# Optimization experiments

Measured on AMD Instinct MI355X. Metric: run time of the kernel, lower is better.

## Reference

```python
import jax, jax.numpy as jnp
import numpy as np

V, D, DEPTH, L, H, DH, FF = 32000, 1024, 4, 2048, 16, 64, 4096
INNER = H * DH
EPS = 1e-5


def ln(x, g, b):
    m = jnp.mean(x, axis=-1, keepdims=True)
    v = jnp.mean(jnp.square(x - m), axis=-1, keepdims=True)
    return (x - m) * jax.lax.rsqrt(v + EPS) * g + b


def setup_inputs() -> dict:
    key = jax.random.key(0)
    ks = jax.random.split(key, 16)
    s = 0.02
    inp = {
        'x': jax.random.randint(ks[0], (1, L), 0, V),
        'tok_emb': jax.random.normal(ks[1], (V, D), jnp.float32) * s,
        'pos_emb': jax.random.normal(ks[2], (L, D), jnp.float32) * s,
        'attn_ng': jnp.ones((DEPTH, D), jnp.float32),
        'attn_nb': jnp.zeros((DEPTH, D), jnp.float32),
        'wqkv': jax.random.normal(ks[3], (DEPTH, D, 3 * INNER), jnp.float32) * s,
        'wo': jax.random.normal(ks[4], (DEPTH, INNER, D), jnp.float32) * s,
        'bo': jnp.zeros((DEPTH, D), jnp.float32),
        'out_ng': jnp.ones((DEPTH, D), jnp.float32),
        'out_nb': jnp.zeros((DEPTH, D), jnp.float32),
        'ff_ng': jnp.ones((DEPTH, D), jnp.float32),
        'ff_nb': jnp.zeros((DEPTH, D), jnp.float32),
        'w1': jax.random.normal(ks[5], (DEPTH, D, FF), jnp.float32) * s,
        'b1': jnp.zeros((DEPTH, FF), jnp.float32),
        'w2': jax.random.normal(ks[6], (DEPTH, FF, D), jnp.float32) * s,
        'b2': jnp.zeros((DEPTH, D), jnp.float32),
        'fin_g': jnp.ones((D,), jnp.float32),
        'fin_b': jnp.zeros((D,), jnp.float32),
        'w_logit': jax.random.normal(ks[7], (D, V), jnp.float32) * s,
        'b_logit': jnp.zeros((V,), jnp.float32),
    }
    return inp


def reference(x, tok_emb, pos_emb, attn_ng, attn_nb, wqkv, wo, bo, out_ng, out_nb,
              ff_ng, ff_nb, w1, b1, w2, b2, fin_g, fin_b, w_logit, b_logit):
    n = x.shape[1]
    scale = DH ** -0.5
    # causal keep-mask: j <= i (lower triangular incl diagonal)
    causal = jnp.tril(jnp.ones((n, n), bool))
    h = tok_emb[x] + pos_emb[:n][None]  # [b, n, D]
    for l in range(DEPTH):
        # --- ReLA attention ---
        y = ln(h, attn_ng[l], attn_nb[l])
        qkv = y @ wqkv[l]  # [b, n, 3*INNER]
        q, k, v = jnp.split(qkv, 3, axis=-1)
        q = q.reshape(-1, n, H, DH).transpose(0, 2, 1, 3) * scale  # [b,H,n,d]
        k = k.reshape(-1, n, H, DH).transpose(0, 2, 1, 3)
        v = v.reshape(-1, n, H, DH).transpose(0, 2, 1, 3)
        sim = jnp.einsum('bhid,bhjd->bhij', q, k)
        attn = jnp.where(causal, jax.nn.relu(sim), 0.0)  # mask then ReLU
        o = jnp.einsum('bhij,bhjd->bhid', attn, v)
        o = o.transpose(0, 2, 1, 3).reshape(-1, n, INNER)  # [b,n,INNER]
        o = ln(o @ wo[l] + bo[l], out_ng[l], out_nb[l])
        h = o + h
        # --- FFN ---
        y = ln(h, ff_ng[l], ff_nb[l])
        y = jax.nn.gelu(y @ w1[l] + b1[l], approximate=False) @ w2[l] + b2[l]
        h = y + h
    return ln(h, fin_g, fin_b) @ w_logit + b_logit
```

## Files before the change

kernel.cpp:

```cpp
#include <hip/hip_runtime.h>
#include <hip/hip_bf16.h>
#include <math.h>

#define SEQ   2048
#define DM    1024
#define NH    16
#define DHD   64
#define FFD   4096
#define NV    32000

typedef __bf16 bf16x8 __attribute__((ext_vector_type(8)));
typedef float  f32x4  __attribute__((ext_vector_type(4)));

typedef __attribute__((address_space(1))) void* gas_ptr;
typedef __attribute__((address_space(3))) void* las_ptr;

static __device__ __forceinline__ void gload16(const void* g, void* l) {
  __builtin_amdgcn_global_load_lds((gas_ptr)g, (las_ptr)l, 16, 0, 0);
}

static __device__ __forceinline__ unsigned short f2bf(float f) {
  unsigned int x = __float_as_uint(f);
  return (unsigned short)((x + 0x7fffu + ((x >> 16) & 1u)) >> 16);
}

static __device__ __forceinline__ bf16x8 ld_frag(const unsigned short* p) {
  union { uint4 u; bf16x8 v; } r;
  r.u = *(const uint4*)p;
  return r.v;
}

__global__ __launch_bounds__(256)
void k_transpose_bf16(const float* __restrict__ in, unsigned short* __restrict__ out,
                      int K, int N, size_t lstride) {
  in  += (size_t)blockIdx.z * lstride;
  out += (size_t)blockIdx.z * lstride;
  __shared__ float tl[64 * 65];
  const int bk = blockIdx.x * 64, bn = blockIdx.y * 64;
  const int t = threadIdx.x;
  const int tx = t & 15, ty = t >> 4;
#pragma unroll
  for (int i = 0; i < 4; ++i) {
    const int r = i * 16 + ty;
    float4 v = *(const float4*)&in[(size_t)(bk + r) * N + bn + tx * 4];
    tl[(tx * 4 + 0) * 65 + r] = v.x;
    tl[(tx * 4 + 1) * 65 + r] = v.y;
    tl[(tx * 4 + 2) * 65 + r] = v.z;
    tl[(tx * 4 + 3) * 65 + r] = v.w;
  }
  __syncthreads();
#pragma unroll
  for (int j = 0; j < 2; ++j) {
    const int f = j * 256 + t;
    const int n = f >> 3, kc = (f & 7) * 8;
    union { unsigned short u[8]; uint4 v; } pk;
#pragma unroll
    for (int e = 0; e < 8; ++e) pk.u[e] = f2bf(tl[n * 65 + kc + e]);
    *(uint4*)&out[(size_t)(bn + n) * K + bk + kc] = pk.v;
  }
}

__global__ __launch_bounds__(256)
void k_vT(const unsigned short* __restrict__ qkv, unsigned short* __restrict__ vT) {
  __shared__ unsigned short tile[32][33];
  const int bs = blockIdx.x * 32, bd = blockIdx.y * 32;
  const int tx = threadIdx.x & 31, ty = threadIdx.x >> 5;
#pragma unroll
  for (int r = ty; r < 32; r += 8)
    tile[r][tx] = qkv[(size_t)(bs + r) * (3 * DM) + 2 * DM + bd + tx];
  __syncthreads();
#pragma unroll
  for (int r = ty; r < 32; r += 8)
    vT[(size_t)(bd + r) * SEQ + bs + tx] = tile[tx][r];
}

__global__ __launch_bounds__(256)
void k_embed(const int* __restrict__ x, const float* __restrict__ tok,
             const float* __restrict__ pos, float* __restrict__ h) {
  const int row = blockIdx.x;
  const int d = threadIdx.x * 4;
  const int tk = x[row];
  float4 a = *(const float4*)(tok + (size_t)tk * DM + d);
  float4 p = *(const float4*)(pos + (size_t)row * DM + d);
  float4 o; o.x = a.x + p.x; o.y = a.y + p.y; o.z = a.z + p.z; o.w = a.w + p.w;
  *(float4*)(h + (size_t)row * DM + d) = o;
}

__global__ __launch_bounds__(256)
void k_ln_bf16(const float* __restrict__ in, const float* __restrict__ g,
               const float* __restrict__ b, unsigned short* __restrict__ out) {
  const int row = blockIdx.x, t = threadIdx.x;
  float4 v = *(const float4*)(in + (size_t)row * DM + t * 4);
  float s = v.x + v.y + v.z + v.w;
  float q = v.x * v.x + v.y * v.y + v.z * v.z + v.w * v.w;
#pragma unroll
  for (int o = 32; o; o >>= 1) { s += __shfl_xor(s, o); q += __shfl_xor(q, o); }
  __shared__ float ls[4], lq[4];
  if ((t & 63) == 0) { ls[t >> 6] = s; lq[t >> 6] = q; }
  __syncthreads();
  s = ls[0] + ls[1] + ls[2] + ls[3];
  q = lq[0] + lq[1] + lq[2] + lq[3];
  const float mean = s * (1.f / DM);
  const float rstd = rsqrtf(q * (1.f / DM) - mean * mean + 1e-5f);
  float4 gg = *(const float4*)(g + t * 4);
  float4 bb = *(const float4*)(b + t * 4);
  ushort4 o4;
  o4.x = f2bf((v.x - mean) * rstd * gg.x + bb.x);
  o4.y = f2bf((v.y - mean) * rstd * gg.y + bb.y);
  o4.z = f2bf((v.z - mean) * rstd * gg.z + bb.z);
  o4.w = f2bf((v.w - mean) * rstd * gg.w + bb.w);
  *(ushort4*)(out + (size_t)row * DM + t * 4) = o4;
}

__global__ __launch_bounds__(256)
void k_addslab_ln_ln(float* __restrict__ h, const float* __restrict__ sl,
                     const float* __restrict__ bo,
                     const float* __restrict__ g1, const float* __restrict__ b1,
                     const float* __restrict__ g2, const float* __restrict__ b2,
                     unsigned short* __restrict__ out) {
  const int row = blockIdx.x, t = threadIdx.x;
  __shared__ float ls[4], lq[4], ls2[4], lq2[4];
  const size_t idx = (size_t)row * DM + t * 4;
  float4 v = *(const float4*)(bo + t * 4);
#pragma unroll
  for (int c = 0; c < 4; ++c) {
    float4 p = *(const float4*)(sl + (size_t)c * SEQ * DM + idx);
    v.x += p.x; v.y += p.y; v.z += p.z; v.w += p.w;
  }
  float s = v.x + v.y + v.z + v.w;
  float q = v.x * v.x + v.y * v.y + v.z * v.z + v.w * v.w;
#pragma unroll
  for (int o = 32; o; o >>= 1) { s += __shfl_xor(s, o); q += __shfl_xor(q, o); }
  if ((t & 63) == 0) { ls[t >> 6] = s; lq[t >> 6] = q; }
  __syncthreads();
  s = ls[0] + ls[1] + ls[2] + ls[3];
  q = lq[0] + lq[1] + lq[2] + lq[3];
  const float mean = s * (1.f / DM);
  const float rstd = rsqrtf(q * (1.f / DM) - mean * mean + 1e-5f);
  float4 gg = *(const float4*)(g1 + t * 4);
  float4 bb = *(const float4*)(b1 + t * 4);
  float4 hv = *(const float4*)(h + idx);
  hv.x += (v.x - mean) * rstd * gg.x + bb.x;
  hv.y += (v.y - mean) * rstd * gg.y + bb.y;
  hv.z += (v.z - mean) * rstd * gg.z + bb.z;
  hv.w += (v.w - mean) * rstd * gg.w + bb.w;
  *(float4*)(h + idx) = hv;
  float s2 = hv.x + hv.y + hv.z + hv.w;
  float q2 = hv.x * hv.x + hv.y * hv.y + hv.z * hv.z + hv.w * hv.w;
#pragma unroll
  for (int o = 32; o; o >>= 1) { s2 += __shfl_xor(s2, o); q2 += __shfl_xor(q2, o); }
  if ((t & 63) == 0) { ls2[t >> 6] = s2; lq2[t >> 6] = q2; }
  __syncthreads();
  s2 = ls2[0] + ls2[1] + ls2[2] + ls2[3];
  q2 = lq2[0] + lq2[1] + lq2[2] + lq2[3];
  const float mean2 = s2 * (1.f / DM);
  const float rstd2 = rsqrtf(q2 * (1.f / DM) - mean2 * mean2 + 1e-5f);
  float4 g2v = *(const float4*)(g2 + t * 4);
  float4 b2v = *(const float4*)(b2 + t * 4);
  ushort4 o4;
  o4.x = f2bf((hv.x - mean2) * rstd2 * g2v.x + b2v.x);
  o4.y = f2bf((hv.y - mean2) * rstd2 * g2v.y + b2v.y);
  o4.z = f2bf((hv.z - mean2) * rstd2 * g2v.z + b2v.z);
  o4.w = f2bf((hv.w - mean2) * rstd2 * g2v.w + b2v.w);
  *(ushort4*)(out + (size_t)row * DM + t * 4) = o4;
}

__global__ __launch_bounds__(256)
void k_redadd_ln(float* __restrict__ h, const float* __restrict__ sl,
                 const float* __restrict__ b2,
                 const float* __restrict__ g, const float* __restrict__ b,
                 unsigned short* __restrict__ out) {
  const int row = blockIdx.x, t = threadIdx.x;
  __shared__ float ls[4], lq[4];
  const size_t idx = (size_t)row * DM + t * 4;
  float4 hv = *(const float4*)(h + idx);
  float4 bb = *(const float4*)(b2 + t * 4);
  hv.x += bb.x; hv.y += bb.y; hv.z += bb.z; hv.w += bb.w;
#pragma unroll
  for (int c = 0; c < 4; ++c) {
    float4 p = *(const float4*)(sl + (size_t)c * SEQ * DM + idx);
    hv.x += p.x; hv.y += p.y; hv.z += p.z; hv.w += p.w;
  }
  *(float4*)(h + idx) = hv;
  float s = hv.x + hv.y + hv.z + hv.w;
  float q = hv.x * hv.x + hv.y * hv.y + hv.z * hv.z + hv.w * hv.w;
#pragma unroll
  for (int o = 32; o; o >>= 1) { s += __shfl_xor(s, o); q += __shfl_xor(q, o); }
  if ((t & 63) == 0) { ls[t >> 6] = s; lq[t >> 6] = q; }
  __syncthreads();
  s = ls[0] + ls[1] + ls[2] + ls[3];
  q = lq[0] + lq[1] + lq[2] + lq[3];
  const float mean = s * (1.f / DM);
  const float rstd = rsqrtf(q * (1.f / DM) - mean * mean + 1e-5f);
  float4 gg = *(const float4*)(g + t * 4);
  float4 b1 = *(const float4*)(b + t * 4);
  ushort4 o4;
  o4.x = f2bf((hv.x - mean) * rstd * gg.x + b1.x);
  o4.y = f2bf((hv.y - mean) * rstd * gg.y + b1.y);
  o4.z = f2bf((hv.z - mean) * rstd * gg.z + b1.z);
  o4.w = f2bf((hv.w - mean) * rstd * gg.w + b1.w);
  *(ushort4*)(out + (size_t)row * DM + t * 4) = o4;
}

template<int EPI>
__global__ __launch_bounds__(512, 1)
void k_gemm2(const unsigned short* __restrict__ A, const unsigned short* __restrict__ Bt,
             float* __restrict__ outF, unsigned short* __restrict__ outB,
             const float* __restrict__ bias, int N, int K, int kLen, int gm) {
  __shared__ __align__(16) unsigned short L[49152];
  const int nwg = gridDim.x, pid = blockIdx.x;
  const int qq = nwg >> 3, rr = nwg & 7;
  const int xcd = pid & 7, lo = pid >> 3;
  const int wg = ((xcd < rr) ? xcd * (qq + 1) : rr * (qq + 1) + (xcd - rr) * qq) + lo;
  const int bm = wg % gm, bn = wg / gm;
  const int kOff = blockIdx.y * kLen;
  const int t = threadIdx.x, lane = t & 63, w = t >> 6;
  const int wm = w >> 2, wn = w & 3, lr = lane & 15, lg = lane >> 4;

  const unsigned short* gA[2]; unsigned short* lA[2];
  const unsigned short* gB[4]; unsigned short* lB[4];
#pragma unroll
  for (int j = 0; j < 2; ++j) {
    const int f = j * 512 + t, row = f >> 3, c = f & 7;
    gA[j] = A + (size_t)(bm * 128 + row) * K + kOff + ((c ^ (row & 7)) << 3);
    lA[j] = L + f * 8;
  }
#pragma unroll
  for (int j = 0; j < 4; ++j) {
    const int f = j * 512 + t, row = f >> 3, c = f & 7;
    gB[j] = Bt + (size_t)(bn * 256 + row) * K + kOff + ((c ^ (row & 7)) << 3);
    lB[j] = L + 16384 + f * 8;
  }
  auto stage = [&](int k0, int c) {
#pragma unroll
    for (int j = 0; j < 2; ++j) gload16(gA[j] + k0, lA[j] + c * 8192);
#pragma unroll
    for (int j = 0; j < 4; ++j) gload16(gB[j] + k0, lB[j] + c * 16384);
  };

  int offA[4][2], offB[4][2];
#pragma unroll
  for (int mt = 0; mt < 4; ++mt)
#pragma unroll
    for (int ks = 0; ks < 2; ++ks) {
      const int rowA = wm * 64 + mt * 16 + lr;
      offA[mt][ks] = rowA * 64 + (((ks * 4 + lg) ^ (rowA & 7)) << 3);
      const int rowB = wn * 64 + mt * 16 + lr;
      offB[mt][ks] = rowB * 64 + (((ks * 4 + lg) ^ (rowB & 7)) << 3);
    }

  const f32x4 zero = {0.f, 0.f, 0.f, 0.f};
  f32x4 acc[4][4];
#pragma unroll
  for (int i = 0; i < 4; ++i)
#pragma unroll
    for (int j = 0; j < 4; ++j) acc[i][j] = zero;

  const int NT = kLen >> 6;
  stage(0, 0);
  if (NT > 1) stage(64, 1);

  for (int tt = 0; tt < NT; ++tt) {
    const int c = tt & 1;
    if (tt + 1 < NT) asm volatile("s_waitcnt vmcnt(6)" ::: "memory");
    else             asm volatile("s_waitcnt vmcnt(0)" ::: "memory");
    __builtin_amdgcn_s_barrier();
    const unsigned short* Ab = L + c * 8192;
    const unsigned short* Bb = L + 16384 + c * 16384;
    bf16x8 af[4][2], bfr[4][2];
#pragma unroll
    for (int mt = 0; mt < 4; ++mt)
#pragma unroll
      for (int ks = 0; ks < 2; ++ks) {
        af[mt][ks]  = ld_frag(Ab + offA[mt][ks]);
        bfr[mt][ks] = ld_frag(Bb + offB[mt][ks]);
      }
    __builtin_amdgcn_s_setprio(1);
#pragma unroll
    for (int ks = 0; ks < 2; ++ks)
#pragma unroll
      for (int mt = 0; mt < 4; ++mt)
#pragma unroll
        for (int nt = 0; nt < 4; ++nt)
          acc[mt][nt] = __builtin_amdgcn_mfma_f32_16x16x32_bf16(af[mt][ks], bfr[nt][ks], acc[mt][nt], 0, 0, 0);
    __builtin_amdgcn_s_setprio(0);
    __builtin_amdgcn_s_barrier();
    if (tt + 2 < NT) stage((tt + 2) << 6, c);
  }

  const int rbase = bm * 128 + wm * 64;
  const int cbase = bn * 256 + wn * 64;
  float* outP = outF;
  if constexpr (EPI == 4) outP = outF + (size_t)blockIdx.y * SEQ * N;
#pragma unroll
  for (int mt = 0; mt < 4; ++mt) {
#pragma unroll
    for (int nt = 0; nt < 4; ++nt) {
      const int col = cbase + nt * 16 + lr;
      float bv = 0.f;
      if constexpr (EPI == 1 || EPI == 2) bv = bias[col];
#pragma unroll
      for (int r = 0; r < 4; ++r) {
        const int row = rbase + mt * 16 + lg * 4 + r;
        float v = acc[mt][nt][r] + bv;
        if constexpr (EPI == 2) v = 0.5f * v * (1.f + erff(v * 0.70710678118f));
        if constexpr (EPI == 0 || EPI == 2) outB[(size_t)row * N + col] = f2bf(v);
        else                                outP[(size_t)row * N + col] = v;
      }
    }
  }
}

__global__ __launch_bounds__(256)
void k_gemm4(const unsigned short* __restrict__ A, const unsigned short* __restrict__ Bt,
             float* __restrict__ outF, const float* __restrict__ bias,
             int N, int K, int gm) {
  __shared__ __align__(16) unsigned short L[16384];
  const int nwg = gridDim.x, pid = blockIdx.x;
  const int qq = nwg >> 3, rr = nwg & 7;
  const int xcd = pid & 7, lo = pid >> 3;
  const int wg = ((xcd < rr) ? xcd * (qq + 1) : rr * (qq + 1) + (xcd - rr) * qq) + lo;
  const int bm = wg % gm, bn = wg / gm;
  const int t = threadIdx.x, lane = t & 63, w = t >> 6;
  const int wm = w >> 1, wn = w & 1, lr = lane & 15, lg = lane >> 4;

  const unsigned short* gA[2]; const unsigned short* gB[2];
  unsigned short* lA[2]; unsigned short* lB[2];
#pragma unroll
  for (int j = 0; j < 2; ++j) {
    const int f = j * 256 + t;
    const int row = f >> 2;
    const int c = (f & 3) ^ (row & 3);
    gA[j] = A  + (size_t)(bm * 128 + row) * K + c * 8;
    gB[j] = Bt + (size_t)(bn * 128 + row) * K + c * 8;
    lA[j] = L + f * 8;
    lB[j] = L + 4096 + f * 8;
  }
  auto stage = [&](int k0, int cb) {
#pragma unroll
    for (int j = 0; j < 2; ++j) gload16(gA[j] + k0, lA[j] + cb * 8192);
#pragma unroll
    for (int j = 0; j < 2; ++j) gload16(gB[j] + k0, lB[j] + cb * 8192);
  };

  int offA[4], offB[4];
#pragma unroll
  for (int mt = 0; mt < 4; ++mt) {
    const int rowA = wm * 64 + mt * 16 + lr;
    offA[mt] = rowA * 32 + ((lg ^ (rowA & 3)) << 3);
    const int rowB = wn * 64 + mt * 16 + lr;
    offB[mt] = 4096 + rowB * 32 + ((lg ^ (rowB & 3)) << 3);
  }

  f32x4 acc[4][4];
#pragma unroll
  for (int i = 0; i < 4; ++i)
#pragma unroll
    for (int j = 0; j < 4; ++j) acc[i][j] = (f32x4){0.f, 0.f, 0.f, 0.f};

  const int NT = K >> 5;
  stage(0, 0);
  stage(32, 1);

  for (int tt = 0; tt < NT; ++tt) {
    const int cb = tt & 1;
    if (tt + 1 < NT) asm volatile("s_waitcnt vmcnt(4)" ::: "memory");
    else             asm volatile("s_waitcnt vmcnt(0)" ::: "memory");
    __builtin_amdgcn_s_barrier();
    const unsigned short* buf = L + cb * 8192;
    bf16x8 af[4], bfr[4];
#pragma unroll
    for (int mt = 0; mt < 4; ++mt) {
      af[mt]  = ld_frag(buf + offA[mt]);
      bfr[mt] = ld_frag(buf + offB[mt]);
    }
    __builtin_amdgcn_s_setprio(1);
#pragma unroll
    for (int mt = 0; mt < 4; ++mt)
#pragma unroll
      for (int nt = 0; nt < 4; ++nt)
        acc[mt][nt] = __builtin_amdgcn_mfma_f32_16x16x32_bf16(af[mt], bfr[nt], acc[mt][nt], 0, 0, 0);
    __builtin_amdgcn_s_setprio(0);
    __builtin_amdgcn_s_barrier();
    if (tt + 2 < NT) stage((tt + 2) << 5, cb);
  }

  const int rbase = bm * 128 + wm * 64;
  const int cbase = bn * 128 + wn * 64;
#pragma unroll
  for (int mt = 0; mt < 4; ++mt) {
#pragma unroll
    for (int nt = 0; nt < 4; ++nt) {
      const int col = cbase + nt * 16 + lr;
      const float bv = bias[col];
#pragma unroll
      for (int r = 0; r < 4; ++r) {
        const int row = rbase + mt * 16 + lg * 4 + r;
        outF[(size_t)row * N + col] = acc[mt][nt][r] + bv;
      }
    }
  }
}

__global__ __launch_bounds__(256)
void k_rela_attn(const unsigned short* __restrict__ qkv,
                 const unsigned short* __restrict__ vT,
                 unsigned short* __restrict__ obf) {
  const int jb = blockIdx.x;
  const int hd = blockIdx.y;
  const int qbA = jb, qbB = 31 - jb;
  const int t = threadIdx.x, lane = t & 63, w = t >> 6;
  const int lr = lane & 15, lg = lane >> 4;

  __shared__ __align__(16) unsigned short Qs[128 * 64];
  __shared__ __align__(16) unsigned short Ks[64 * 64];
  __shared__ __align__(16) unsigned short Vs[64 * 64];
  __shared__ __align__(16) unsigned short Ps[4][16 * 72];

  const int sr8 = lane >> 3;
  const int sch = ((lane & 7) ^ sr8) << 3;

#pragma unroll
  for (int qi = 0; qi < 4; ++qi) {
    const int i = w * 4 + qi;
    const int rl = i * 8 + sr8;
    const int grow = (rl < 64) ? (qbA * 64 + rl) : (qbB * 64 + rl - 64);
    gload16(qkv + (size_t)grow * (3 * DM) + hd * DHD + sch, Qs + i * 512);
  }
  __syncthreads();

  bf16x8 qfA[2], qfB[2];
#pragma unroll
  for (int ks = 0; ks < 2; ++ks) {
    const int rowA = w * 16 + lr;
    qfA[ks] = ld_frag(&Qs[rowA * 64 + (((ks * 4 + lg) ^ (lr & 7)) << 3)]);
    const int rowB = 64 + w * 16 + lr;
    qfB[ks] = ld_frag(&Qs[rowB * 64 + (((ks * 4 + lg) ^ (lr & 7)) << 3)]);
  }

  const f32x4 zero = {0.f, 0.f, 0.f, 0.f};
  f32x4 accA[4], accB[4];
#pragma unroll
  for (int nt = 0; nt < 4; ++nt) { accA[nt] = zero; accB[nt] = zero; }

  auto tile_step = [&](const bf16x8* qf, f32x4* acc, int qb, int kt) {
    f32x4 sv[4];
#pragma unroll
    for (int nt = 0; nt < 4; ++nt) sv[nt] = zero;
#pragma unroll
    for (int ks = 0; ks < 2; ++ks)
#pragma unroll
      for (int nt = 0; nt < 4; ++nt) {
        bf16x8 kf = ld_frag(&Ks[(nt * 16 + lr) * 64 + (((ks * 4 + lg) ^ (lr & 7)) << 3)]);
        sv[nt] = __builtin_amdgcn_mfma_f32_16x16x32_bf16(qf[ks], kf, sv[nt], 0, 0, 0);
      }
    const bool diag = (kt == qb);
#pragma unroll
    for (int nt = 0; nt < 4; ++nt)
#pragma unroll
      for (int r = 0; r < 4; ++r) {
        float v = fmaxf(sv[nt][r], 0.f) * 0.125f;
        if (diag) {
          const int ii = w * 16 + lg * 4 + r;
          const int jj = nt * 16 + lr;
          if (jj > ii) v = 0.f;
        }
        Ps[w][(lg * 4 + r) * 72 + nt * 16 + lr] = f2bf(v);
      }
#pragma unroll
    for (int ks = 0; ks < 2; ++ks) {
      bf16x8 pf = ld_frag(&Ps[w][lr * 72 + ks * 32 + lg * 8]);
#pragma unroll
      for (int nt = 0; nt < 4; ++nt) {
        bf16x8 vf = ld_frag(&Vs[(nt * 16 + lr) * 64 + (((ks * 4 + lg) ^ (lr & 7)) << 3)]);
        acc[nt] = __builtin_amdgcn_mfma_f32_16x16x32_bf16(pf, vf, acc[nt], 0, 0, 0);
      }
    }
  };

  for (int kt = 0; kt <= qbB; ++kt) {
    __syncthreads();
#pragma unroll
    for (int qi = 0; qi < 2; ++qi) {
      const int i = w * 2 + qi;
      const int rl = i * 8 + sr8;
      gload16(qkv + (size_t)(kt * 64 + rl) * (3 * DM) + DM + hd * DHD + sch, Ks + i * 512);
      gload16(vT + (size_t)(hd * DHD + rl) * SEQ + kt * 64 + sch, Vs + i * 512);
    }
    __syncthreads();
    tile_step(qfB, accB, qbB, kt);
    if (kt <= qbA) tile_step(qfA, accA, qbA, kt);
  }

#pragma unroll
  for (int nt = 0; nt < 4; ++nt)
#pragma unroll
    for (int r = 0; r < 4; ++r) {
      const int col = hd * DHD + nt * 16 + lr;
      const int rowA = qbA * 64 + w * 16 + lg * 4 + r;
      obf[(size_t)rowA * DM + col] = f2bf(accA[nt][r]);
      const int rowB = qbB * 64 + w * 16 + lg * 4 + r;
      obf[(size_t)rowB * DM + col] = f2bf(accB[nt][r]);
    }
}

extern "C" void kernel_launch(void* const* d_in, const int* in_sizes, int n_in,
                              void* d_out, int out_size, void* d_ws, size_t ws_size,
                              hipStream_t stream) {
  const int*   x       = (const int*)d_in[0];
  const float* tok_emb = (const float*)d_in[1];
  const float* pos_emb = (const float*)d_in[2];
  const float* attn_ng = (const float*)d_in[3];
  const float* attn_nb = (const float*)d_in[4];
  const float* wqkv    = (const float*)d_in[5];
  const float* wo      = (const float*)d_in[6];
  const float* bo      = (const float*)d_in[7];
  const float* out_ng  = (const float*)d_in[8];
  const float* out_nb  = (const float*)d_in[9];
  const float* ff_ng   = (const float*)d_in[10];
  const float* ff_nb   = (const float*)d_in[11];
  const float* w1      = (const float*)d_in[12];
  const float* b1      = (const float*)d_in[13];
  const float* w2      = (const float*)d_in[14];
  const float* b2      = (const float*)d_in[15];
  const float* fin_g   = (const float*)d_in[16];
  const float* fin_b   = (const float*)d_in[17];
  const float* w_logit = (const float*)d_in[18];
  const float* b_logit = (const float*)d_in[19];
  float* out = (float*)d_out;

  char* ws = (char*)d_ws;
  size_t off = 0;
  auto alloc = [&](size_t bytes) -> void* {
    void* p = ws + off;
    off = (off + bytes + 255) & ~(size_t)255;
    return p;
  };
  unsigned short* wqkvT = (unsigned short*)alloc(4ull * 3072 * 1024 * 2);
  unsigned short* woT   = (unsigned short*)alloc(4ull * 1024 * 1024 * 2);
  unsigned short* w1T   = (unsigned short*)alloc(4ull * 4096 * 1024 * 2);
  unsigned short* w2T   = (unsigned short*)alloc(4ull * 1024 * 4096 * 2);
  unsigned short* wlogT = (unsigned short*)alloc((size_t)NV * 1024 * 2);
  float*          h     = (float*)alloc((size_t)SEQ * DM * 4);
  unsigned short* ybf   = (unsigned short*)alloc((size_t)SEQ * DM * 2);
  unsigned short* qkvbf = (unsigned short*)alloc((size_t)SEQ * 3 * DM * 2);
  unsigned short* vTb   = (unsigned short*)alloc((size_t)DM * SEQ * 2);
  unsigned short* obf   = (unsigned short*)alloc((size_t)SEQ * DM * 2);
  unsigned short* ffbf  = (unsigned short*)alloc((size_t)SEQ * FFD * 2);
  float*          slabs = (float*)alloc(4ull * SEQ * DM * 4);
  (void)ws_size; (void)in_sizes; (void)n_in; (void)out_size;

  const dim3 B(256);
  const dim3 G2(512);

  k_transpose_bf16<<<dim3(16, 48, 4), B, 0, stream>>>(wqkv, wqkvT, 1024, 3072, (size_t)1024 * 3072);
  k_transpose_bf16<<<dim3(16, 16, 4), B, 0, stream>>>(wo, woT, 1024, 1024, (size_t)1024 * 1024);
  k_transpose_bf16<<<dim3(16, 64, 4), B, 0, stream>>>(w1, w1T, 1024, 4096, (size_t)1024 * 4096);
  k_transpose_bf16<<<dim3(64, 16, 4), B, 0, stream>>>(w2, w2T, 4096, 1024, (size_t)4096 * 1024);
  k_transpose_bf16<<<dim3(16, 500, 1), B, 0, stream>>>(w_logit, wlogT, 1024, NV, 0);

  k_embed<<<SEQ, B, 0, stream>>>(x, tok_emb, pos_emb, h);
  k_ln_bf16<<<SEQ, B, 0, stream>>>(h, attn_ng, attn_nb, ybf);

  for (int l = 0; l < 4; ++l) {
    k_gemm2<0><<<dim3(192), G2, 0, stream>>>(
        ybf, wqkvT + (size_t)l * 3072 * 1024, nullptr, qkvbf, nullptr, 3072, 1024, 1024, 16);
    k_vT<<<dim3(SEQ / 32, DM / 32), B, 0, stream>>>(qkvbf, vTb);
    k_rela_attn<<<dim3(16, NH), B, 0, stream>>>(qkvbf, vTb, obf);
    k_gemm2<4><<<dim3(64, 4), G2, 0, stream>>>(
        obf, woT + (size_t)l * 1024 * 1024, slabs, nullptr, nullptr, 1024, 1024, 256, 16);
    k_addslab_ln_ln<<<SEQ, B, 0, stream>>>(h, slabs, bo + l * DM,
                                           out_ng + l * DM, out_nb + l * DM,
                                           ff_ng + l * DM, ff_nb + l * DM, ybf);
    k_gemm2<2><<<dim3(256), G2, 0, stream>>>(
        ybf, w1T + (size_t)l * 4096 * 1024, nullptr, ffbf, b1 + l * FFD, 4096, 1024, 1024, 16);
    k_gemm2<4><<<dim3(64, 4), G2, 0, stream>>>(
        ffbf, w2T + (size_t)l * 1024 * 4096, slabs, nullptr, nullptr, 1024, 4096, 1024, 16);
    const float* ng = (l < 3) ? (attn_ng + (l + 1) * DM) : fin_g;
    const float* nb = (l < 3) ? (attn_nb + (l + 1) * DM) : fin_b;
    k_redadd_ln<<<SEQ, B, 0, stream>>>(h, slabs, b2 + l * DM, ng, nb, ybf);
  }

  k_gemm4<<<dim3(4000), B, 0, stream>>>(ybf, wlogT, out, b_logit, NV, 1024, 16);
}
```

Before: 1.028 ms.

## Unify GEMMs on 128x128 tile kernel and split attention KV range across two blocks

Replaces the 512-thread 128x256 GEMM with a templated 256-thread 128x128 kernel (BK=32, new swizzle) used by every layer GEMM and the logit projection. The attention kernel is split along the key dimension into two z-slices with double-buffered K/V staging. Each slice writes fp32 partial outputs, and a new kernel sums them into bf16. This aims to balance work and raise occupancy, at the cost of an extra reduction kernel, fp32 slab traffic, and smaller GEMM tiles with less reuse.

```diff
diff --git a/kernel.cpp b/kernel.cpp
--- a/kernel.cpp
+++ b/kernel.cpp
@@ -110,6 +110,20 @@
   o4.z = f2bf((v.z - mean) * rstd * gg.z + bb.z);
   o4.w = f2bf((v.w - mean) * rstd * gg.w + bb.w);
   *(ushort4*)(out + (size_t)row * DM + t * 4) = o4;
+}
+
+__global__ __launch_bounds__(256)
+void k_ored(const float* __restrict__ sl, unsigned short* __restrict__ obf) {
+  const int row = blockIdx.x, t = threadIdx.x;
+  const size_t idx = (size_t)row * DM + t * 4;
+  float4 a = *(const float4*)(sl + idx);
+  float4 b = *(const float4*)(sl + (size_t)SEQ * DM + idx);
+  ushort4 o4;
+  o4.x = f2bf(a.x + b.x);
+  o4.y = f2bf(a.y + b.y);
+  o4.z = f2bf(a.z + b.z);
+  o4.w = f2bf(a.w + b.w);
+  *(ushort4*)(obf + idx) = o4;
 }
 
 __global__ __launch_bounds__(256)
@@ -203,11 +217,11 @@
 }
 
 template<int EPI>
-__global__ __launch_bounds__(512, 1)
-void k_gemm2(const unsigned short* __restrict__ A, const unsigned short* __restrict__ Bt,
+__global__ __launch_bounds__(256)
+void k_gemm4(const unsigned short* __restrict__ A, const unsigned short* __restrict__ Bt,
              float* __restrict__ outF, unsigned short* __restrict__ outB,
              const float* __restrict__ bias, int N, int K, int kLen, int gm) {
-  __shared__ __align__(16) unsigned short L[49152];
+  __shared__ __align__(16) unsigned short L[16384];
   const int nwg = gridDim.x, pid = blockIdx.x;
   const int qq = nwg >> 3, rr = nwg & 7;
   const int xcd = pid & 7, lo = pid >> 3;
@@ -215,81 +229,71 @@
   const int bm = wg % gm, bn = wg / gm;
   const int kOff = blockIdx.y * kLen;
   const int t = threadIdx.x, lane = t & 63, w = t >> 6;
-  const int wm = w >> 2, wn = w & 3, lr = lane & 15, lg = lane >> 4;
-
-  const unsigned short* gA[2]; unsigned short* lA[2];
-  const unsigned short* gB[4]; unsigned short* lB[4];
+  const int wm = w >> 1, wn = w & 1, lr = lane & 15, lg = lane >> 4;
+
+  const unsigned short* gA[2]; const unsigned short* gB[2];
+  unsigned short* lA[2]; unsigned short* lB[2];
 #pragma unroll
   for (int j = 0; j < 2; ++j) {
-    const int f = j * 512 + t, row = f >> 3, c = f & 7;
-    gA[j] = A + (size_t)(bm * 128 + row) * K + kOff + ((c ^ (row & 7)) << 3);
+    const int f = j * 256 + t;
+    const int row = f >> 2;
+    const int c = (f & 3) ^ ((row >> 1) & 3);
+    gA[j] = A  + (size_t)(bm * 128 + row) * K + kOff + c * 8;
+    gB[j] = Bt + (size_t)(bn * 128 + row) * K + kOff + c * 8;
     lA[j] = L + f * 8;
-  }
-#pragma unroll
-  for (int j = 0; j < 4; ++j) {
-    const int f = j * 512 + t, row = f >> 3, c = f & 7;
-    gB[j] = Bt + (size_t)(bn * 256 + row) * K + kOff + ((c ^ (row & 7)) << 3);
-    lB[j] = L + 16384 + f * 8;
-  }
-  auto stage = [&](int k0, int c) {
-#pragma unroll
-    for (int j = 0; j < 2; ++j) gload16(gA[j] + k0, lA[j] + c * 8192);
-#pragma unroll
-    for (int j = 0; j < 4; ++j) gload16(gB[j] + k0, lB[j] + c * 16384);
+    lB[j] = L + 4096 + f * 8;
+  }
+  auto stage = [&](int k0, int cb) {
+#pragma unroll
+    for (int j = 0; j < 2; ++j) gload16(gA[j] + k0, lA[j] + cb * 8192);
+#pragma unroll
+    for (int j = 0; j < 2; ++j) gload16(gB[j] + k0, lB[j] + cb * 8192);
   };
 
-  int offA[4][2], offB[4][2];
-#pragma unroll
-  for (int mt = 0; mt < 4; ++mt)
-#pragma unroll
-    for (int ks = 0; ks < 2; ++ks) {
-      const int rowA = wm * 64 + mt * 16 + lr;
-      offA[mt][ks] = rowA * 64 + (((ks * 4 + lg) ^ (rowA & 7)) << 3);
-      const int rowB = wn * 64 + mt * 16 + lr;
-      offB[mt][ks] = rowB * 64 + (((ks * 4 + lg) ^ (rowB & 7)) << 3);
-    }
-
-  const f32x4 zero = {0.f, 0.f, 0.f, 0.f};
+  int offA[4], offB[4];
+#pragma unroll
+  for (int mt = 0; mt < 4; ++mt) {
+    const int rowA = wm * 64 + mt * 16 + lr;
+    offA[mt] = rowA * 32 + ((lg ^ ((rowA >> 1) & 3)) << 3);
+    const int rowB = wn * 64 + mt * 16 + lr;
+    offB[mt] = 4096 + rowB * 32 + ((lg ^ ((rowB >> 1) & 3)) << 3);
+  }
+
   f32x4 acc[4][4];
 #pragma unroll
   for (int i = 0; i < 4; ++i)
 #pragma unroll
-    for (int j = 0; j < 4; ++j) acc[i][j] = zero;
-
-  const int NT = kLen >> 6;
+    for (int j = 0; j < 4; ++j) acc[i][j] = (f32x4){0.f, 0.f, 0.f, 0.f};
+
+  const int NT = kLen >> 5;
   stage(0, 0);
-  if (NT > 1) stage(64, 1);
+  stage(32, 1);
 
   for (int tt = 0; tt < NT; ++tt) {
-    const int c = tt & 1;
-    if (tt + 1 < NT) asm volatile("s_waitcnt vmcnt(6)" ::: "memory");
+    const int cb = tt & 1;
+    if (tt + 1 < NT) asm volatile("s_waitcnt vmcnt(4)" ::: "memory");
     else             asm volatile("s_waitcnt vmcnt(0)" ::: "memory");
     __builtin_amdgcn_s_barrier();
-    const unsigned short* Ab = L + c * 8192;
-    const unsigned short* Bb = L + 16384 + c * 16384;
-    bf16x8 af[4][2], bfr[4][2];
+    const unsigned short* buf = L + cb * 8192;
+    bf16x8 af[4], bfr[4];
+#pragma unroll
+    for (int mt = 0; mt < 4; ++mt) {
+      af[mt]  = ld_frag(buf + offA[mt]);
+      bfr[mt] = ld_frag(buf + offB[mt]);
+    }
+    __builtin_amdgcn_s_setprio(1);
 #pragma unroll
     for (int mt = 0; mt < 4; ++mt)
 #pragma unroll
-      for (int ks = 0; ks < 2; ++ks) {
-        af[mt][ks]  = ld_frag(Ab + offA[mt][ks]);
-        bfr[mt][ks] = ld_frag(Bb + offB[mt][ks]);
-      }
-    __builtin_amdgcn_s_setprio(1);
-#pragma unroll
-    for (int ks = 0; ks < 2; ++ks)
-#pragma unroll
-      for (int mt = 0; mt < 4; ++mt)
-#pragma unroll
-        for (int nt = 0; nt < 4; ++nt)
-          acc[mt][nt] = __builtin_amdgcn_mfma_f32_16x16x32_bf16(af[mt][ks], bfr[nt][ks], acc[mt][nt], 0, 0, 0);
+      for (int nt = 0; nt < 4; ++nt)
+        acc[mt][nt] = __builtin_amdgcn_mfma_f32_16x16x32_bf16(af[mt], bfr[nt], acc[mt][nt], 0, 0, 0);
     __builtin_amdgcn_s_setprio(0);
     __builtin_amdgcn_s_barrier();
-    if (tt + 2 < NT) stage((tt + 2) << 6, c);
+    if (tt + 2 < NT) stage((tt + 2) << 5, cb);
   }
 
   const int rbase = bm * 128 + wm * 64;
-  const int cbase = bn * 256 + wn * 64;
+  const int cbase = bn * 128 + wn * 64;
   float* outP = outF;
   if constexpr (EPI == 4) outP = outF + (size_t)blockIdx.y * SEQ * N;
 #pragma unroll
@@ -312,109 +316,20 @@
 }
 
 __global__ __launch_bounds__(256)
-void k_gemm4(const unsigned short* __restrict__ A, const unsigned short* __restrict__ Bt,
-             float* __restrict__ outF, const float* __restrict__ bias,
-             int N, int K, int gm) {
-  __shared__ __align__(16) unsigned short L[16384];
-  const int nwg = gridDim.x, pid = blockIdx.x;
-  const int qq = nwg >> 3, rr = nwg & 7;
-  const int xcd = pid & 7, lo = pid >> 3;
-  const int wg = ((xcd < rr) ? xcd * (qq + 1) : rr * (qq + 1) + (xcd - rr) * qq) + lo;
-  const int bm = wg % gm, bn = wg / gm;
-  const int t = threadIdx.x, lane = t & 63, w = t >> 6;
-  const int wm = w >> 1, wn = w & 1, lr = lane & 15, lg = lane >> 4;
-
-  const unsigned short* gA[2]; const unsigned short* gB[2];
-  unsigned short* lA[2]; unsigned short* lB[2];
-#pragma unroll
-  for (int j = 0; j < 2; ++j) {
-    const int f = j * 256 + t;
-    const int row = f >> 2;
-    const int c = (f & 3) ^ (row & 3);
-    gA[j] = A  + (size_t)(bm * 128 + row) * K + c * 8;
-    gB[j] = Bt + (size_t)(bn * 128 + row) * K + c * 8;
-    lA[j] = L + f * 8;
-    lB[j] = L + 4096 + f * 8;
-  }
-  auto stage = [&](int k0, int cb) {
-#pragma unroll
-    for (int j = 0; j < 2; ++j) gload16(gA[j] + k0, lA[j] + cb * 8192);
-#pragma unroll
-    for (int j = 0; j < 2; ++j) gload16(gB[j] + k0, lB[j] + cb * 8192);
-  };
-
-  int offA[4], offB[4];
-#pragma unroll
-  for (int mt = 0; mt < 4; ++mt) {
-    const int rowA = wm * 64 + mt * 16 + lr;
-    offA[mt] = rowA * 32 + ((lg ^ (rowA & 3)) << 3);
-    const int rowB = wn * 64 + mt * 16 + lr;
-    offB[mt] = 4096 + rowB * 32 + ((lg ^ (rowB & 3)) << 3);
-  }
-
-  f32x4 acc[4][4];
-#pragma unroll
-  for (int i = 0; i < 4; ++i)
-#pragma unroll
-    for (int j = 0; j < 4; ++j) acc[i][j] = (f32x4){0.f, 0.f, 0.f, 0.f};
-
-  const int NT = K >> 5;
-  stage(0, 0);
-  stage(32, 1);
-
-  for (int tt = 0; tt < NT; ++tt) {
-    const int cb = tt & 1;
-    if (tt + 1 < NT) asm volatile("s_waitcnt vmcnt(4)" ::: "memory");
-    else             asm volatile("s_waitcnt vmcnt(0)" ::: "memory");
-    __builtin_amdgcn_s_barrier();
-    const unsigned short* buf = L + cb * 8192;
-    bf16x8 af[4], bfr[4];
-#pragma unroll
-    for (int mt = 0; mt < 4; ++mt) {
-      af[mt]  = ld_frag(buf + offA[mt]);
-      bfr[mt] = ld_frag(buf + offB[mt]);
-    }
-    __builtin_amdgcn_s_setprio(1);
-#pragma unroll
-    for (int mt = 0; mt < 4; ++mt)
-#pragma unroll
-      for (int nt = 0; nt < 4; ++nt)
-        acc[mt][nt] = __builtin_amdgcn_mfma_f32_16x16x32_bf16(af[mt], bfr[nt], acc[mt][nt], 0, 0, 0);
-    __builtin_amdgcn_s_setprio(0);
-    __builtin_amdgcn_s_barrier();
-    if (tt + 2 < NT) stage((tt + 2) << 5, cb);
-  }
-
-  const int rbase = bm * 128 + wm * 64;
-  const int cbase = bn * 128 + wn * 64;
-#pragma unroll
-  for (int mt = 0; mt < 4; ++mt) {
-#pragma unroll
-    for (int nt = 0; nt < 4; ++nt) {
-      const int col = cbase + nt * 16 + lr;
-      const float bv = bias[col];
-#pragma unroll
-      for (int r = 0; r < 4; ++r) {
-        const int row = rbase + mt * 16 + lg * 4 + r;
-        outF[(size_t)row * N + col] = acc[mt][nt][r] + bv;
-      }
-    }
-  }
-}
-
-__global__ __launch_bounds__(256)
 void k_rela_attn(const unsigned short* __restrict__ qkv,
                  const unsigned short* __restrict__ vT,
-                 unsigned short* __restrict__ obf) {
+                 float* __restrict__ osl) {
   const int jb = blockIdx.x;
   const int hd = blockIdx.y;
+  const int z  = blockIdx.z;
   const int qbA = jb, qbB = 31 - jb;
+  const int ha = (qbA + 2) >> 1, hb = (qbB + 2) >> 1;
   const int t = threadIdx.x, lane = t & 63, w = t >> 6;
   const int lr = lane & 15, lg = lane >> 4;
 
   __shared__ __align__(16) unsigned short Qs[128 * 64];
-  __shared__ __align__(16) unsigned short Ks[64 * 64];
-  __shared__ __align__(16) unsigned short Vs[64 * 64];
+  __shared__ __align__(16) unsigned short Ks[2][64 * 64];
+  __shared__ __align__(16) unsigned short Vs[2][64 * 64];
   __shared__ __align__(16) unsigned short Ps[4][16 * 72];
 
   const int sr8 = lane >> 3;
@@ -443,7 +358,17 @@
 #pragma unroll
   for (int nt = 0; nt < 4; ++nt) { accA[nt] = zero; accB[nt] = zero; }
 
-  auto tile_step = [&](const bf16x8* qf, f32x4* acc, int qb, int kt) {
+  auto stage = [&](int kt, int cb) {
+#pragma unroll
+    for (int qi = 0; qi < 2; ++qi) {
+      const int i = w * 2 + qi;
+      const int rl = i * 8 + sr8;
+      gload16(qkv + (size_t)(kt * 64 + rl) * (3 * DM) + DM + hd * DHD + sch, &Ks[cb][i * 512]);
+      gload16(vT + (size_t)(hd * DHD + rl) * SEQ + kt * 64 + sch, &Vs[cb][i * 512]);
+    }
+  };
+
+  auto tile_step = [&](const bf16x8* qf, f32x4* acc, int qb, int kt, int cb) {
     f32x4 sv[4];
 #pragma unroll
     for (int nt = 0; nt < 4; ++nt) sv[nt] = zero;
@@ -451,7 +376,7 @@
     for (int ks = 0; ks < 2; ++ks)
 #pragma unroll
       for (int nt = 0; nt < 4; ++nt) {
-        bf16x8 kf = ld_frag(&Ks[(nt * 16 + lr) * 64 + (((ks * 4 + lg) ^ (lr & 7)) << 3)]);
+        bf16x8 kf = ld_frag(&Ks[cb][(nt * 16 + lr) * 64 + (((ks * 4 + lg) ^ (lr & 7)) << 3)]);
         sv[nt] = __builtin_amdgcn_mfma_f32_16x16x32_bf16(qf[ks], kf, sv[nt], 0, 0, 0);
       }
     const bool diag = (kt == qb);
@@ -472,35 +397,47 @@
       bf16x8 pf = ld_frag(&Ps[w][lr * 72 + ks * 32 + lg * 8]);
 #pragma unroll
       for (int nt = 0; nt < 4; ++nt) {
-        bf16x8 vf = ld_frag(&Vs[(nt * 16 + lr) * 64 + (((ks * 4 + lg) ^ (lr & 7)) << 3)]);
+        bf16x8 vf = ld_frag(&Vs[cb][(nt * 16 + lr) * 64 + (((ks * 4 + lg) ^ (lr & 7)) << 3)]);
         acc[nt] = __builtin_amdgcn_mfma_f32_16x16x32_bf16(pf, vf, acc[nt], 0, 0, 0);
       }
     }
   };
 
-  for (int kt = 0; kt <= qbB; ++kt) {
-    __syncthreads();
-#pragma unroll
-    for (int qi = 0; qi < 2; ++qi) {
-      const int i = w * 2 + qi;
-      const int rl = i * 8 + sr8;
-      gload16(qkv + (size_t)(kt * 64 + rl) * (3 * DM) + DM + hd * DHD + sch, Ks + i * 512);
-      gload16(vT + (size_t)(hd * DHD + rl) * SEQ + kt * 64 + sch, Vs + i * 512);
+  auto run = [&](int beg, int end, int mode) {
+    if (beg >= end) return;
+    stage(beg, 0);
+    for (int kt = beg; kt < end; ++kt) {
+      const int cb = (kt - beg) & 1;
+      if (kt + 1 < end) {
+        stage(kt + 1, cb ^ 1);
+        asm volatile("s_waitcnt vmcnt(4)" ::: "memory");
+      } else {
+        asm volatile("s_waitcnt vmcnt(0)" ::: "memory");
+      }
+      __builtin_amdgcn_s_barrier();
+      if (mode != 1) tile_step(qfB, accB, qbB, kt, cb);
+      if (mode == 1 || (mode == 0 && kt < ha)) tile_step(qfA, accA, qbA, kt, cb);
+      __builtin_amdgcn_s_barrier();
     }
-    __syncthreads();
-    tile_step(qfB, accB, qbB, kt);
-    if (kt <= qbA) tile_step(qfA, accA, qbA, kt);
-  }
-
+  };
+
+  if (z == 0) {
+    run(0, hb, 0);
+  } else {
+    run(ha, qbA + 1, 1);
+    run(hb, qbB + 1, 2);
+  }
+
+  float* op = osl + (size_t)z * SEQ * DM;
 #pragma unroll
   for (int nt = 0; nt < 4; ++nt)
 #pragma unroll
     for (int r = 0; r < 4; ++r) {
       const int col = hd * DHD + nt * 16 + lr;
       const int rowA = qbA * 64 + w * 16 + lg * 4 + r;
-      obf[(size_t)rowA * DM + col] = f2bf(accA[nt][r]);
+      op[(size_t)rowA * DM + col] = accA[nt][r];
       const int rowB = qbB * 64 + w * 16 + lg * 4 + r;
-      obf[(size_t)rowB * DM + col] = f2bf(accB[nt][r]);
+      op[(size_t)rowB * DM + col] = accB[nt][r];
     }
 }
 
@@ -551,7 +488,6 @@
   (void)ws_size; (void)in_sizes; (void)n_in; (void)out_size;
 
   const dim3 B(256);
-  const dim3 G2(512);
 
   k_transpose_bf16<<<dim3(16, 48, 4), B, 0, stream>>>(wqkv, wqkvT, 1024, 3072, (size_t)1024 * 3072);
   k_transpose_bf16<<<dim3(16, 16, 4), B, 0, stream>>>(wo, woT, 1024, 1024, (size_t)1024 * 1024);
@@ -563,23 +499,24 @@
   k_ln_bf16<<<SEQ, B, 0, stream>>>(h, attn_ng, attn_nb, ybf);
 
   for (int l = 0; l < 4; ++l) {
-    k_gemm2<0><<<dim3(192), G2, 0, stream>>>(
+    k_gemm4<0><<<dim3(384), B, 0, stream>>>(
         ybf, wqkvT + (size_t)l * 3072 * 1024, nullptr, qkvbf, nullptr, 3072, 1024, 1024, 16);
     k_vT<<<dim3(SEQ / 32, DM / 32), B, 0, stream>>>(qkvbf, vTb);
-    k_rela_attn<<<dim3(16, NH), B, 0, stream>>>(qkvbf, vTb, obf);
-    k_gemm2<4><<<dim3(64, 4), G2, 0, stream>>>(
+    k_rela_attn<<<dim3(16, NH, 2), B, 0, stream>>>(qkvbf, vTb, slabs);
+    k_ored<<<SEQ, B, 0, stream>>>(slabs, obf);
+    k_gemm4<4><<<dim3(128, 4), B, 0, stream>>>(
         obf, woT + (size_t)l * 1024 * 1024, slabs, nullptr, nullptr, 1024, 1024, 256, 16);
     k_addslab_ln_ln<<<SEQ, B, 0, stream>>>(h, slabs, bo + l * DM,
                                            out_ng + l * DM, out_nb + l * DM,
                                            ff_ng + l * DM, ff_nb + l * DM, ybf);
-    k_gemm2<2><<<dim3(256), G2, 0, stream>>>(
+    k_gemm4<2><<<dim3(512), B, 0, stream>>>(
         ybf, w1T + (size_t)l * 4096 * 1024, nullptr, ffbf, b1 + l * FFD, 4096, 1024, 1024, 16);
-    k_gemm2<4><<<dim3(64, 4), G2, 0, stream>>>(
+    k_gemm4<4><<<dim3(128, 4), B, 0, stream>>>(
         ffbf, w2T + (size_t)l * 1024 * 4096, slabs, nullptr, nullptr, 1024, 4096, 1024, 16);
     const float* ng = (l < 3) ? (attn_ng + (l + 1) * DM) : fin_g;
     const float* nb = (l < 3) ? (attn_nb + (l + 1) * DM) : fin_b;
     k_redadd_ln<<<SEQ, B, 0, stream>>>(h, slabs, b2 + l * DM, ng, nb, ybf);
   }
 
-  k_gemm4<<<dim3(4000), B, 0, stream>>>(ybf, wlogT, out, b_logit, NV, 1024, 16);
-}
+  k_gemm4<1><<<dim3(4000), B, 0, stream>>>(ybf, wlogT, out, nullptr, b_logit, NV, 1024, 1024, 16);
+}
```

Result: no change. 1.025 ms (-0.4%).
